# Kernel tuning notes

Measured on AMD Instinct MI355X. Metric: run time of the kernel, lower is better.

Reference implementation:

```python
import jax, jax.numpy as jnp
import numpy as np

B, S, D, H = 2, 2048, 1024, 16
HD = D // H  # 64
NEG = 1.0e9


def setup_inputs() -> dict:
    key = jax.random.key(0)
    ks = jax.random.split(key, 9)
    scale = 1.0 / np.sqrt(D)
    return {
        "q_in": jax.random.normal(ks[0], (B, S, D), jnp.float32),
        "k_in": jax.random.normal(ks[1], (B, S, D), jnp.float32),
        "v_in": jax.random.normal(ks[2], (B, S, D), jnp.float32),
        "Wq": jax.random.normal(ks[3], (D, D), jnp.float32) * scale,
        "bq": jnp.zeros((D,), jnp.float32),
        "Wk": jax.random.normal(ks[4], (D, D), jnp.float32) * scale,
        "bk": jnp.zeros((D,), jnp.float32),
        "Wv": jax.random.normal(ks[5], (D, D), jnp.float32) * scale,
        "bv": jnp.zeros((D,), jnp.float32),
        "Wo": jax.random.normal(ks[6], (D, D), jnp.float32) * scale,
        "bo": jnp.zeros((D,), jnp.float32),
    }


def _split_heads(x):
    # [B,S,D] -> [B,H,S,HD]
    return x.reshape(B, S, H, HD).transpose(0, 2, 1, 3)


def reference(q_in, k_in, v_in, Wq, bq, Wk, bk, Wv, bv, Wo, bo):
    q = _split_heads(q_in @ Wq + bq)
    k = _split_heads(k_in @ Wk + bk)
    v = _split_heads(v_in @ Wv + bv)
    # scaled dot-product attention with additive causal mask (use_causal_mask=True)
    scores = jnp.einsum("bhqd,bhkd->bhqk", q, k) / jnp.sqrt(jnp.float32(HD))
    causal = jnp.tril(jnp.ones((S, S), jnp.float32))  # band_part(ones, -1, 0)
    scores = scores + (causal - 1.0) * NEG
    weights = jax.nn.softmax(scores, axis=-1)
    attn = jnp.einsum("bhqk,bhkd->bhqd", weights, v)
    concat = attn.transpose(0, 2, 1, 3).reshape(B, S, D)
    return concat @ Wo + bo
```

## Files before the change

kernel.cpp:

```cpp
#include <hip/hip_runtime.h>

#define B_  2
#define S_  2048
#define D_  1024
#define H_  16
#define HD_ 64
#define MM  (B_ * S_)

typedef __bf16 bf16;
typedef __attribute__((ext_vector_type(8))) __bf16 bf16x8;
typedef __attribute__((ext_vector_type(4))) __bf16 bf16x4;
typedef __attribute__((ext_vector_type(4))) float  f32x4;

__device__ inline float exp2g(float x) { return __builtin_amdgcn_exp2f(x); }

__device__ inline bf16x8 load8(const bf16* p) { return *(const bf16x8*)p; }
__device__ inline bf16x8 load8(const float* p) {
  float4 a = *(const float4*)p;
  float4 b = *(const float4*)(p + 4);
  bf16x8 r;
  r[0] = (bf16)a.x; r[1] = (bf16)a.y; r[2] = (bf16)a.z; r[3] = (bf16)a.w;
  r[4] = (bf16)b.x; r[5] = (bf16)b.y; r[6] = (bf16)b.z; r[7] = (bf16)b.w;
  return r;
}

__device__ inline void gld16(void* lds, const void* g) {
  __builtin_amdgcn_global_load_lds(
      (const __attribute__((address_space(1))) unsigned int*)g,
      (__attribute__((address_space(3))) unsigned int*)lds, 16, 0, 0);
}

__global__ __launch_bounds__(256) void transpose_w(
    const float* __restrict__ W0, const float* __restrict__ W1,
    const float* __restrict__ W2, const float* __restrict__ W3,
    bf16* __restrict__ T0, bf16* __restrict__ T1,
    bf16* __restrict__ T2, bf16* __restrict__ T3,
    const float* __restrict__ X0, const float* __restrict__ X1,
    const float* __restrict__ X2,
    bf16* __restrict__ Y0, bf16* __restrict__ Y1, bf16* __restrict__ Y2) {
  const int z = blockIdx.z;
  if (z >= 4) {
    const int p = z - 4, t = p >> 2;
    const float* src = t == 0 ? X0 : t == 1 ? X1 : X2;
    bf16* dst = t == 0 ? Y0 : t == 1 ? Y1 : Y2;
    long base = ((long)(p & 3) << 20) +
                (long)(blockIdx.y * 32 + blockIdx.x) * 1024 + threadIdx.x * 4;
    float4 v = *(const float4*)&src[base];
    bf16x4 o4;
    o4[0] = (bf16)v.x; o4[1] = (bf16)v.y; o4[2] = (bf16)v.z; o4[3] = (bf16)v.w;
    *(bf16x4*)&dst[base] = o4;
    return;
  }
  __shared__ bf16 t[32][40];
  const float* in = z == 0 ? W0 : z == 1 ? W1 : z == 2 ? W2 : W3;
  bf16* out = z == 0 ? T0 : z == 1 ? T1 : z == 2 ? T2 : T3;
  const int tx = threadIdx.x & 31;
  const int ty = threadIdx.x >> 5;
  const int r0 = blockIdx.y * 32, c0 = blockIdx.x * 32;
#pragma unroll
  for (int j = 0; j < 32; j += 8)
    t[ty + j][tx] = (bf16)in[(long)(r0 + ty + j) * D_ + (c0 + tx)];
  __syncthreads();
#pragma unroll
  for (int j = 0; j < 32; j += 8)
    out[(long)(c0 + ty + j) * D_ + (r0 + tx)] = t[tx][ty + j];
}

__global__ __launch_bounds__(256) void transpose_v64(const bf16* __restrict__ V,
                                                     bf16* __restrict__ VT) {
  __shared__ bf16 t[64][72];
  const int tid = threadIdx.x;
  const int s0 = blockIdx.x * 64;
  const int bh = blockIdx.y;
  const int b = bh >> 4, h = bh & 15;
  const bf16* ip = V + (long)b * S_ * D_ + h * HD_;
  bf16* op = VT + (long)bh * HD_ * S_;
#pragma unroll
  for (int i = 0; i < 2; ++i) {
    int c = tid + i * 256;
    int r = c >> 3, cc = (c & 7) * 8;
    *(bf16x8*)&t[r][cc] = *(const bf16x8*)&ip[(long)(s0 + r) * D_ + cc];
  }
  __syncthreads();
#pragma unroll
  for (int i = 0; i < 2; ++i) {
    int c = tid + i * 256;
    int d = c >> 3, sc = (c & 7) * 8;
    bf16x8 v;
#pragma unroll
    for (int j = 0; j < 8; ++j) v[j] = t[sc + j][d];
    *(bf16x8*)&op[(long)d * S_ + s0 + sc] = v;
  }
}

template <typename AT, typename OT>
__global__ __launch_bounds__(256) void gemm_bt_dma(
    const AT* __restrict__ A0, const AT* __restrict__ A1, const AT* __restrict__ A2,
    const bf16* __restrict__ B0, const bf16* __restrict__ B1, const bf16* __restrict__ B2,
    const float* __restrict__ c0, const float* __restrict__ c1, const float* __restrict__ c2,
    OT* __restrict__ C0, OT* __restrict__ C1, OT* __restrict__ C2,
    int M, int N, int K) {
  __shared__ bf16 lA[2][128][32];
  __shared__ bf16 lB[2][128][32];
  const int z = blockIdx.z;
  const AT*    A    = z == 0 ? A0 : z == 1 ? A1 : A2;
  const bf16*  Bt   = z == 0 ? B0 : z == 1 ? B1 : B2;
  const float* bias = z == 0 ? c0 : z == 1 ? c1 : c2;
  OT*          C    = z == 0 ? C0 : z == 1 ? C1 : C2;

  const int tid = threadIdx.x;
  const int lane = tid & 63, wave = tid >> 6;
  const int quad = lane >> 4, l16 = lane & 15;
  const int bm = blockIdx.y * 128, bn = blockIdx.x * 128;
  const int wm = (wave >> 1) * 64, wn = (wave & 1) * 64;

  f32x4 acc[4][4] = {};

  for (int k0 = 0; k0 < K; k0 += 64) {
    __syncthreads();
#pragma unroll
    for (int hh = 0; hh < 2; ++hh) {
#pragma unroll
      for (int i = 0; i < 2; ++i) {
        const int nbase = wave * 128 + i * 64;
        const int n = nbase + lane;
        const int row = n >> 2, kc = (n & 3) * 8;
        gld16(&lB[hh][0][0] + (long)nbase * 8,
              &Bt[(long)(bn + row) * K + k0 + hh * 32 + kc]);
        if constexpr (__is_same(AT, bf16))
          gld16(&lA[hh][0][0] + (long)nbase * 8,
                &A[(long)(bm + row) * K + k0 + hh * 32 + kc]);
      }
      if constexpr (!__is_same(AT, bf16)) {
#pragma unroll
        for (int i = 0; i < 2; ++i) {
          int c = tid + i * 256;
          int row = c >> 2, kc = (c & 3) * 8;
          *(bf16x8*)&lA[hh][row][kc] =
              load8(&A[(long)(bm + row) * K + k0 + hh * 32 + kc]);
        }
      }
    }
    __syncthreads();
#pragma unroll
    for (int hh = 0; hh < 2; ++hh) {
      bf16x8 af[4], bfr[4];
#pragma unroll
      for (int i = 0; i < 4; ++i) {
        af[i]  = *(const bf16x8*)&lA[hh][wm + i * 16 + l16][quad * 8];
        bfr[i] = *(const bf16x8*)&lB[hh][wn + i * 16 + l16][quad * 8];
      }
#pragma unroll
      for (int mi = 0; mi < 4; ++mi)
#pragma unroll
        for (int ni = 0; ni < 4; ++ni)
          acc[mi][ni] = __builtin_amdgcn_mfma_f32_16x16x32_bf16(
              af[mi], bfr[ni], acc[mi][ni], 0, 0, 0);
    }
  }

#pragma unroll
  for (int mi = 0; mi < 4; ++mi)
#pragma unroll
    for (int ni = 0; ni < 4; ++ni) {
      int col = bn + wn + ni * 16 + l16;
      float bv = bias[col];
#pragma unroll
      for (int r = 0; r < 4; ++r) {
        int row = bm + wm + mi * 16 + quad * 4 + r;
        C[(long)row * N + col] = (OT)(acc[mi][ni][r] + bv);
      }
    }
}

__global__ __launch_bounds__(256) void gemm_bt_64(const bf16* __restrict__ A,
                                                  const bf16* __restrict__ Bt,
                                                  const float* __restrict__ bias,
                                                  float* __restrict__ C,
                                                  int M, int N, int K) {
  __shared__ bf16 lA[2][128][32];
  __shared__ bf16 lB[2][64][32];
  const int tid = threadIdx.x;
  const int lane = tid & 63, wave = tid >> 6;
  const int quad = lane >> 4, l16 = lane & 15;
  const int bm = blockIdx.y * 128, bn = blockIdx.x * 64;
  const int wm = (wave >> 1) * 64, wn = (wave & 1) * 32;

  f32x4 acc[4][2] = {};

  for (int k0 = 0; k0 < K; k0 += 64) {
    __syncthreads();
#pragma unroll
    for (int hh = 0; hh < 2; ++hh) {
#pragma unroll
      for (int i = 0; i < 2; ++i) {
        const int nbase = wave * 128 + i * 64;
        const int n = nbase + lane;
        const int row = n >> 2, kc = (n & 3) * 8;
        gld16(&lA[hh][0][0] + (long)nbase * 8,
              &A[(long)(bm + row) * K + k0 + hh * 32 + kc]);
      }
      {
        const int nbase = wave * 64;
        const int n = nbase + lane;
        const int row = n >> 2, kc = (n & 3) * 8;
        gld16(&lB[hh][0][0] + (long)nbase * 8,
              &Bt[(long)(bn + row) * K + k0 + hh * 32 + kc]);
      }
    }
    __syncthreads();
#pragma unroll
    for (int hh = 0; hh < 2; ++hh) {
      bf16x8 af[4], bfr[2];
#pragma unroll
      for (int i = 0; i < 4; ++i)
        af[i] = *(const bf16x8*)&lA[hh][wm + i * 16 + l16][quad * 8];
#pragma unroll
      for (int i = 0; i < 2; ++i)
        bfr[i] = *(const bf16x8*)&lB[hh][wn + i * 16 + l16][quad * 8];
#pragma unroll
      for (int mi = 0; mi < 4; ++mi)
#pragma unroll
        for (int ni = 0; ni < 2; ++ni)
          acc[mi][ni] = __builtin_amdgcn_mfma_f32_16x16x32_bf16(
              af[mi], bfr[ni], acc[mi][ni], 0, 0, 0);
    }
  }

#pragma unroll
  for (int mi = 0; mi < 4; ++mi)
#pragma unroll
    for (int ni = 0; ni < 2; ++ni) {
      int col = bn + wn + ni * 16 + l16;
      float bv = bias[col];
#pragma unroll
      for (int r = 0; r < 4; ++r) {
        int row = bm + wm + mi * 16 + quad * 4 + r;
        C[(long)row * N + col] = acc[mi][ni][r] + bv;
      }
    }
}

#define SCALE_LOG2E 0.1803368801111244f

__device__ inline void attn_step5(bool diag, int qloc, int quad, int l16,
                                  const bf16 (*lKb)[64], const bf16 (*lVb)[64],
                                  bf16 (*lpw)[72], const bf16x8* aq,
                                  f32x4* o, float& l_s) {
  const int sw = l16 & 7;
  f32x4 s[4];
#pragma unroll
  for (int ni = 0; ni < 4; ++ni) {
    f32x4 a = {};
#pragma unroll
    for (int c = 0; c < 2; ++c) {
      bf16x8 kf = *(const bf16x8*)&lKb[ni * 16 + l16][((c * 4 + quad) ^ sw) * 8];
      a = __builtin_amdgcn_mfma_f32_16x16x32_bf16(kf, aq[c], a, 0, 0, 0);
    }
    s[ni] = a * SCALE_LOG2E;
  }
  if (diag) {
#pragma unroll
    for (int ni = 0; ni < 4; ++ni)
#pragma unroll
      for (int r = 0; r < 4; ++r)
        if (ni * 16 + quad * 4 + r > qloc) s[ni][r] = -1e9f;
  }
  float rs = 0.f;
#pragma unroll
  for (int ni = 0; ni < 4; ++ni) {
    bf16x4 p4;
#pragma unroll
    for (int r = 0; r < 4; ++r) {
      float p = exp2g(s[ni][r]);
      p4[r] = (bf16)p;
      rs += p;
    }
    *(bf16x4*)&lpw[l16][ni * 16 + quad * 4] = p4;
  }
  l_s += rs;
#pragma unroll
  for (int c = 0; c < 2; ++c) {
    bf16x8 ap = *(const bf16x8*)&lpw[l16][c * 32 + quad * 8];
#pragma unroll
    for (int di = 0; di < 4; ++di) {
      bf16x8 vf = *(const bf16x8*)&lVb[di * 16 + l16][((c * 4 + quad) ^ sw) * 8];
      o[di] = __builtin_amdgcn_mfma_f32_16x16x32_bf16(vf, ap, o[di], 0, 0, 0);
    }
  }
}

__device__ inline void store_o(bf16* Ob, int qrow, int lane, int quad, int l16,
                               bf16 (*lpw)[72], const f32x4* o, float l_s) {
  float rs = l_s;
  rs += __shfl_xor(rs, 16);
  rs += __shfl_xor(rs, 32);
  const float inv = 1.0f / rs;
#pragma unroll
  for (int di = 0; di < 4; ++di) {
    bf16x4 p4;
#pragma unroll
    for (int r = 0; r < 4; ++r) p4[r] = (bf16)(o[di][r] * inv);
    *(bf16x4*)&lpw[l16][di * 16 + quad * 4] = p4;
  }
  const int q = lane >> 2, db = (lane & 3) * 16;
  bf16x8 v0 = *(const bf16x8*)&lpw[q][db];
  bf16x8 v1 = *(const bf16x8*)&lpw[q][db + 8];
  *(bf16x8*)&Ob[(long)(qrow + q) * D_ + db] = v0;
  *(bf16x8*)&Ob[(long)(qrow + q) * D_ + db + 8] = v1;
}

__global__ __launch_bounds__(512) void flash_attn5(const bf16* __restrict__ Q,
                                                   const bf16* __restrict__ K,
                                                   const bf16* __restrict__ VT,
                                                   bf16* __restrict__ O) {
  __shared__ bf16 lK[2][64][64];
  __shared__ bf16 lV[2][64][64];
  __shared__ bf16 lp[8][16][72];
  const int tid = threadIdx.x;
  const int lane = tid & 63, wave = tid >> 6;
  const int quad = lane >> 4, l16 = lane & 15;
  const int x = blockIdx.x, bh = blockIdx.y;
  const int qtA = x, qtB = 31 - x;
  const bool isB = wave >= 4;
  const int w4 = wave & 3;
  const int myqt = isB ? qtB : qtA;
  const int b = bh >> 4, h = bh & 15;
  const bf16* Qb = Q + (long)b * S_ * D_ + h * HD_;
  const bf16* Kb = K + (long)b * S_ * D_ + h * HD_;
  const bf16* Vb = VT + (long)bh * HD_ * S_;
  const int qrow = myqt * 64 + w4 * 16;
  const int qloc = w4 * 16 + l16;

  bf16x8 aq[2];
#pragma unroll
  for (int c = 0; c < 2; ++c)
    aq[c] = *(const bf16x8*)&Qb[(long)(qrow + l16) * D_ + c * 32 + quad * 8];

  f32x4 o[4] = {};
  float l_s = 0.f;

  const int srow = tid >> 3, scol = tid & 7;
  const int swcol = (scol ^ (srow & 7)) * 8;

  bf16x8 kreg, vreg;
  kreg = *(const bf16x8*)&Kb[(long)srow * D_ + scol * 8];
  vreg = *(const bf16x8*)&Vb[(long)srow * S_ + scol * 8];
  *(bf16x8*)&lK[0][srow][swcol] = kreg;
  *(bf16x8*)&lV[0][srow][swcol] = vreg;
  __syncthreads();

  const int ktMax = qtB;
  for (int kt = 0; kt <= ktMax; ++kt) {
    const int p = kt & 1;
    if (kt < ktMax) {
      const long k0 = (long)(kt + 1) * 64;
      kreg = *(const bf16x8*)&Kb[(k0 + srow) * D_ + scol * 8];
      vreg = *(const bf16x8*)&Vb[(long)srow * S_ + k0 + scol * 8];
    }
    if (isB || kt <= qtA)
      attn_step5(kt == myqt, qloc, quad, l16, lK[p], lV[p], lp[wave], aq,
                 o, l_s);
    if (kt < ktMax) {
      *(bf16x8*)&lK[1 - p][srow][swcol] = kreg;
      *(bf16x8*)&lV[1 - p][srow][swcol] = vreg;
      __syncthreads();
    }
  }

  bf16* Ob = O + (long)b * S_ * D_ + h * HD_;
  store_o(Ob, qrow, lane, quad, l16, lp[wave], o, l_s);
}

extern "C" void kernel_launch(void* const* d_in, const int* in_sizes, int n_in,
                              void* d_out, int out_size, void* d_ws, size_t ws_size,
                              hipStream_t stream) {
  (void)in_sizes; (void)n_in; (void)out_size;
  const float* q_in = (const float*)d_in[0];
  const float* k_in = (const float*)d_in[1];
  const float* v_in = (const float*)d_in[2];
  const float* Wq   = (const float*)d_in[3];
  const float* bq   = (const float*)d_in[4];
  const float* Wk   = (const float*)d_in[5];
  const float* bk   = (const float*)d_in[6];
  const float* Wv   = (const float*)d_in[7];
  const float* bv   = (const float*)d_in[8];
  const float* Wo   = (const float*)d_in[9];
  const float* bo   = (const float*)d_in[10];
  float* out = (float*)d_out;

  bf16* ws = (bf16*)d_ws;
  const size_t WSZ = (size_t)D_ * D_;
  const size_t TSZ = (size_t)B_ * S_ * D_;
  bf16* WqT = ws;
  bf16* WkT = WqT + WSZ;
  bf16* WvT = WkT + WSZ;
  bf16* WoT = WvT + WSZ;
  bf16* Qp  = WoT + WSZ;
  bf16* Kp  = Qp + TSZ;
  bf16* Vp  = Kp + TSZ;
  bf16* VTp = Vp + TSZ;
  bf16* Ap  = VTp + TSZ;
  bf16* Xq  = VTp;
  bf16* Xk  = Ap;
  bf16* Xv  = Ap + TSZ;
  const bool pre = ws_size >= (4 * WSZ + 6 * TSZ) * sizeof(bf16);

  dim3 blk(256);
  transpose_w<<<dim3(32, 32, pre ? 16 : 4), blk, 0, stream>>>(
      Wq, Wk, Wv, Wo, WqT, WkT, WvT, WoT, q_in, k_in, v_in, Xq, Xk, Xv);

  if (pre)
    gemm_bt_dma<bf16, bf16><<<dim3(8, 32, 3), blk, 0, stream>>>(
        Xq, Xk, Xv, WqT, WkT, WvT, bq, bk, bv, Qp, Kp, Vp, MM, D_, D_);
  else
    gemm_bt_dma<float, bf16><<<dim3(8, 32, 3), blk, 0, stream>>>(
        q_in, k_in, v_in, WqT, WkT, WvT, bq, bk, bv, Qp, Kp, Vp, MM, D_, D_);

  transpose_v64<<<dim3(S_ / 64, B_ * H_), blk, 0, stream>>>(Vp, VTp);

  flash_attn5<<<dim3(16, B_ * H_), dim3(512), 0, stream>>>(Qp, Kp, VTp, Ap);

  gemm_bt_64<<<dim3(16, 32), blk, 0, stream>>>(Ap, WoT, bo, out, MM, D_, D_);
}
```

Before: 226.7 us.

## Split KV range across wave groups per query tile and merge partial outputs

The attention kernel now gives each block a single query tile and splits its key/value tiles between two groups of four waves (even and odd tiles). Each iteration loads 128 keys, and the partial outputs and row sums are combined through shared memory at the end. The grid doubles to 32x32 blocks, replacing the earlier pairing of a short and a long query tile per block. It also raises wave priority around the MFMA sections. The trade-off is extra synchronisation, a merge step, and single-buffered LDS with two barriers per iteration.

New measurement: 241.6 us. 6.6% more time.

```diff
diff --git a/kernel.cpp b/kernel.cpp
--- a/kernel.cpp
+++ b/kernel.cpp
@@ -243,22 +243,25 @@
 
 #define SCALE_LOG2E 0.1803368801111244f
 
-__device__ inline void attn_step5(bool diag, int qloc, int quad, int l16,
-                                  const bf16 (*lKb)[64], const bf16 (*lVb)[64],
+__device__ inline void attn_step6(bool diag, int qloc, int quad, int l16, int g,
+                                  const bf16 (*lKb)[64], const bf16 (*lVb)[128],
                                   bf16 (*lpw)[72], const bf16x8* aq,
                                   f32x4* o, float& l_s) {
   const int sw = l16 & 7;
   f32x4 s[4];
+  __builtin_amdgcn_s_setprio(1);
 #pragma unroll
   for (int ni = 0; ni < 4; ++ni) {
     f32x4 a = {};
 #pragma unroll
     for (int c = 0; c < 2; ++c) {
-      bf16x8 kf = *(const bf16x8*)&lKb[ni * 16 + l16][((c * 4 + quad) ^ sw) * 8];
+      bf16x8 kf =
+          *(const bf16x8*)&lKb[g * 64 + ni * 16 + l16][((c * 4 + quad) ^ sw) * 8];
       a = __builtin_amdgcn_mfma_f32_16x16x32_bf16(kf, aq[c], a, 0, 0, 0);
     }
     s[ni] = a * SCALE_LOG2E;
   }
+  __builtin_amdgcn_s_setprio(0);
   if (diag) {
 #pragma unroll
     for (int ni = 0; ni < 4; ++ni)
@@ -279,15 +282,18 @@
     *(bf16x4*)&lpw[l16][ni * 16 + quad * 4] = p4;
   }
   l_s += rs;
+  __builtin_amdgcn_s_setprio(1);
 #pragma unroll
   for (int c = 0; c < 2; ++c) {
     bf16x8 ap = *(const bf16x8*)&lpw[l16][c * 32 + quad * 8];
 #pragma unroll
     for (int di = 0; di < 4; ++di) {
-      bf16x8 vf = *(const bf16x8*)&lVb[di * 16 + l16][((c * 4 + quad) ^ sw) * 8];
+      bf16x8 vf =
+          *(const bf16x8*)&lVb[di * 16 + l16][g * 64 + ((c * 4 + quad) ^ sw) * 8];
       o[di] = __builtin_amdgcn_mfma_f32_16x16x32_bf16(vf, ap, o[di], 0, 0, 0);
     }
   }
+  __builtin_amdgcn_s_setprio(0);
 }
 
 __device__ inline void store_o(bf16* Ob, int qrow, int lane, int quad, int l16,
@@ -310,26 +316,28 @@
   *(bf16x8*)&Ob[(long)(qrow + q) * D_ + db + 8] = v1;
 }
 
-__global__ __launch_bounds__(512) void flash_attn5(const bf16* __restrict__ Q,
+__global__ __launch_bounds__(512) void flash_attn6(const bf16* __restrict__ Q,
                                                    const bf16* __restrict__ K,
                                                    const bf16* __restrict__ VT,
                                                    bf16* __restrict__ O) {
-  __shared__ bf16 lK[2][64][64];
-  __shared__ bf16 lV[2][64][64];
+  __shared__ __align__(16) union {
+    struct { bf16 K[128][64]; bf16 VT[64][128]; } s;
+    struct { float o[4][16][68]; float l[4][64]; } m;
+  } u;
   __shared__ bf16 lp[8][16][72];
   const int tid = threadIdx.x;
   const int lane = tid & 63, wave = tid >> 6;
   const int quad = lane >> 4, l16 = lane & 15;
-  const int x = blockIdx.x, bh = blockIdx.y;
-  const int qtA = x, qtB = 31 - x;
+  const int qt = 31 - blockIdx.x;
+  const int bh = blockIdx.y;
   const bool isB = wave >= 4;
+  const int g = isB ? 1 : 0;
   const int w4 = wave & 3;
-  const int myqt = isB ? qtB : qtA;
   const int b = bh >> 4, h = bh & 15;
   const bf16* Qb = Q + (long)b * S_ * D_ + h * HD_;
   const bf16* Kb = K + (long)b * S_ * D_ + h * HD_;
   const bf16* Vb = VT + (long)bh * HD_ * S_;
-  const int qrow = myqt * 64 + w4 * 16;
+  const int qrow = qt * 64 + w4 * 16;
   const int qloc = w4 * 16 + l16;
 
   bf16x8 aq[2];
@@ -340,36 +348,62 @@
   f32x4 o[4] = {};
   float l_s = 0.f;
 
-  const int srow = tid >> 3, scol = tid & 7;
-  const int swcol = (scol ^ (srow & 7)) * 8;
-
-  bf16x8 kreg, vreg;
-  kreg = *(const bf16x8*)&Kb[(long)srow * D_ + scol * 8];
-  vreg = *(const bf16x8*)&Vb[(long)srow * S_ + scol * 8];
-  *(bf16x8*)&lK[0][srow][swcol] = kreg;
-  *(bf16x8*)&lV[0][srow][swcol] = vreg;
+  const int kr0 = tid >> 3, kc0 = tid & 7;
+  const int vr0 = tid >> 4, vc0 = tid & 15;
+  const int ksw = (kc0 ^ (kr0 & 7)) * 8;
+  const int vsw = (((vc0 & 7) ^ (vr0 & 7)) + (vc0 >> 3) * 8) * 8;
+
+  bf16x8 rk0, rk1, rv0, rv1;
+  const int nt = qt + 1;
+  const int nit = (nt + 1) >> 1;
+
+  rk0 = *(const bf16x8*)&Kb[(long)kr0 * D_ + kc0 * 8];
+  rk1 = *(const bf16x8*)&Kb[(long)(kr0 + 64) * D_ + kc0 * 8];
+  rv0 = *(const bf16x8*)&Vb[(long)vr0 * S_ + vc0 * 8];
+  rv1 = *(const bf16x8*)&Vb[(long)(vr0 + 32) * S_ + vc0 * 8];
+  *(bf16x8*)&u.s.K[kr0][ksw] = rk0;
+  *(bf16x8*)&u.s.K[kr0 + 64][ksw] = rk1;
+  *(bf16x8*)&u.s.VT[vr0][vsw] = rv0;
+  *(bf16x8*)&u.s.VT[vr0 + 32][vsw] = rv1;
   __syncthreads();
 
-  const int ktMax = qtB;
-  for (int kt = 0; kt <= ktMax; ++kt) {
-    const int p = kt & 1;
-    if (kt < ktMax) {
-      const long k0 = (long)(kt + 1) * 64;
-      kreg = *(const bf16x8*)&Kb[(k0 + srow) * D_ + scol * 8];
-      vreg = *(const bf16x8*)&Vb[(long)srow * S_ + k0 + scol * 8];
-    }
-    if (isB || kt <= qtA)
-      attn_step5(kt == myqt, qloc, quad, l16, lK[p], lV[p], lp[wave], aq,
+  for (int it = 0; it < nit; ++it) {
+    if (it + 1 < nit) {
+      const long k0 = (long)(it + 1) * 128;
+      rk0 = *(const bf16x8*)&Kb[(k0 + kr0) * D_ + kc0 * 8];
+      rk1 = *(const bf16x8*)&Kb[(k0 + kr0 + 64) * D_ + kc0 * 8];
+      rv0 = *(const bf16x8*)&Vb[(long)vr0 * S_ + k0 + vc0 * 8];
+      rv1 = *(const bf16x8*)&Vb[(long)(vr0 + 32) * S_ + k0 + vc0 * 8];
+    }
+    const int tile = 2 * it + g;
+    if (tile < nt)
+      attn_step6(tile == qt, qloc, quad, l16, g, u.s.K, u.s.VT, lp[wave], aq,
                  o, l_s);
-    if (kt < ktMax) {
-      *(bf16x8*)&lK[1 - p][srow][swcol] = kreg;
-      *(bf16x8*)&lV[1 - p][srow][swcol] = vreg;
+    __syncthreads();
+    if (it + 1 < nit) {
+      *(bf16x8*)&u.s.K[kr0][ksw] = rk0;
+      *(bf16x8*)&u.s.K[kr0 + 64][ksw] = rk1;
+      *(bf16x8*)&u.s.VT[vr0][vsw] = rv0;
+      *(bf16x8*)&u.s.VT[vr0 + 32][vsw] = rv1;
       __syncthreads();
     }
   }
 
-  bf16* Ob = O + (long)b * S_ * D_ + h * HD_;
-  store_o(Ob, qrow, lane, quad, l16, lp[wave], o, l_s);
+  if (isB) {
+#pragma unroll
+    for (int di = 0; di < 4; ++di)
+      *(f32x4*)&u.m.o[w4][l16][di * 16 + quad * 4] = o[di];
+    u.m.l[w4][lane] = l_s;
+  }
+  __syncthreads();
+  if (!isB) {
+    l_s += u.m.l[w4][lane];
+#pragma unroll
+    for (int di = 0; di < 4; ++di)
+      o[di] += *(const f32x4*)&u.m.o[w4][l16][di * 16 + quad * 4];
+    bf16* Ob = O + (long)b * S_ * D_ + h * HD_;
+    store_o(Ob, qrow, lane, quad, l16, lp[wave], o, l_s);
+  }
 }
 
 extern "C" void kernel_launch(void* const* d_in, const int* in_sizes, int n_in,
@@ -419,7 +453,7 @@
 
   transpose_v64<<<dim3(S_ / 64, B_ * H_), blk, 0, stream>>>(Vp, VTp);
 
-  flash_attn5<<<dim3(16, B_ * H_), dim3(512), 0, stream>>>(Qp, Kp, VTp, Ap);
+  flash_attn6<<<dim3(32, B_ * H_), dim3(512), 0, stream>>>(Qp, Kp, VTp, Ap);
 
   gemm_bt_64<<<dim3(16, 32), blk, 0, stream>>>(Ap, WoT, bo, out, MM, D_, D_);
 }
```
